# Performance work log

Measured on AMD Instinct MI355X. Metric: run time of the kernel, lower is better.

The kernel has to match this reference:

```python
import jax, jax.numpy as jnp
import numpy as np

CUTOFF = 4          # lattice cutoff radius (module init arg)
NMAX = 64           # padded max neighbors per mobile site (~58 actual at cutoff=4)
BATCH = 131072      # number of independent configurations
B_SOFT = 0.01       # softening constant b in vint
FAR = 1e6           # padding position, masked out


def _rot(c):
    return np.array([[np.cos(c), -np.sin(c)], [np.sin(c), np.cos(c)]])


def _build_geometry():
    """Replicates PotEnergy1P.__init__ (with the intended, bug-fixed math)."""
    s3 = np.sqrt(3.0)
    base = [np.array([0.5, s3 / 6]), np.array([1.0, -s3 / 3]),
            np.array([1.5, s3 / 6]), np.array([1.0, 2 * s3 / 3])]
    mobile = base \
        + [_rot(2 * np.pi / 3) @ p for p in base] \
        + [_rot(4 * np.pi / 3) @ p for p in base]
    mobile = np.stack(mobile)                      # [12, 2]

    def ntopos(n1, n2):
        return np.array([0.5, s3 / 6]) + n1 * np.array([1.0, 0.0]) \
            + n2 * np.array([-0.5, s3 / 2])

    rng = range(-4 * CUTOFF, 4 * CUTOFF)
    grid = np.array([ntopos(n1, n2) for n1 in rng for n2 in rng])  # [G, 2]
    dist = np.linalg.norm(grid[:, None, :] - mobile[None, :, :], axis=-1)  # [G, 12]
    not_mobile = ~np.any(np.isclose(dist, 0.0, atol=1e-8), axis=1)        # [G]

    neighbors = np.full((12, NMAX, 2), FAR, dtype=np.float32)
    mask = np.zeros((12, NMAX), dtype=np.float32)
    for i in range(12):
        idx = np.where(not_mobile & (dist[:, i] < CUTOFF))[0]
        k = len(idx)
        assert k <= NMAX
        neighbors[i, :k] = grid[idx]
        mask[i, :k] = 1.0
    return neighbors, mask


def setup_inputs() -> dict:
    key = jax.random.key(0)
    x = jax.random.normal(key, (BATCH, 24), dtype=jnp.float32)
    neighbors, mask = _build_geometry()
    return {"x": x,
            "neighbors": jnp.asarray(neighbors),
            "mask": jnp.asarray(mask)}


def reference(x, neighbors, mask):
    # x: [B, 24] -> [B, 12, 2] mobile positions
    xr = x.reshape(x.shape[0], -1, 2)
    # pairwise displacement to all padded neighbors: [B, 12, NMAX, 2]
    d = xr[:, :, None, :] - neighbors[None, :, :, :]
    r = jnp.sqrt(jnp.sum(d * d, axis=-1))          # [B, 12, NMAX]
    v = jnp.exp(-r) / (r + B_SOFT)                 # vint with a=1.0, b=0.01
    return jnp.sum(v * mask[None], axis=(1, 2))    # [B] total potential energy
```

## Files before the change

### kernel.cpp

```cpp
#include <hip/hip_runtime.h>

#define NMAX   64
#define NSITES 12
#define SPLIT  4
#define BLOCK  256
#define ROWS   66

#define LOG2E  1.44269504088896340736f
#define LN2    0.69314718055994530942f
#define B_SOFT 0.01f
#define PAD_C  2.0e6f

__global__ __launch_bounds__(BLOCK, 8)
void pot_energy_kernel(const float* __restrict__ x,
                       const float* __restrict__ neighbors,
                       const float* __restrict__ mask,
                       float* __restrict__ out, int B) {
    __shared__ float2 nb[NSITES * ROWS];
    __shared__ int    cnt[NSITES];

    const int tid  = threadIdx.x;
    const int wv   = tid >> 6;
    const int lane = tid & 63;

    for (int idx = tid; idx < NSITES * ROWS; idx += BLOCK)
        nb[idx] = make_float2(PAD_C, PAD_C);
    __syncthreads();

    for (int s = wv; s < NSITES; s += 4) {
        const bool keep = mask[s * NMAX + lane] > 0.5f;
        const unsigned long long bal = __ballot(keep);
        if (keep) {
            const int pos = __popcll(bal & ((1ull << lane) - 1ull));
            const float2 p = ((const float2*)neighbors)[s * NMAX + lane];
            nb[s * ROWS + pos] = make_float2(p.x * LOG2E, p.y * LOG2E);
        }
        if (lane == 0) cnt[s] = __popcll(bal);
    }
    __syncthreads();

    int m = 0;
    #pragma unroll
    for (int s = 0; s < NSITES; ++s) m = max(m, cnt[s]);
    m = (__builtin_amdgcn_readfirstlane(m) + 3) & ~3;

    const int gtid = blockIdx.x * BLOCK + tid;
    const int e = gtid >> 2;
    const int q = gtid & 3;
    if (e >= B) return;

    const float2* xp = (const float2*)(x + (size_t)gtid * 6);
    const float2 p0 = xp[0], p1 = xp[1], p2 = xp[2];
    const float xs_[3] = { p0.x * LOG2E, p1.x * LOG2E, p2.x * LOG2E };
    const float ys_[3] = { p0.y * LOG2E, p1.y * LOG2E, p2.y * LOG2E };

    float acc0 = 0.f, acc1 = 0.f;
    #pragma unroll
    for (int s = 0; s < 3; ++s) {
        const int site = q * 3 + s;
        const float xs = xs_[s];
        const float ys = ys_[s];
        const float4* __restrict__ row4 = (const float4*)&nb[site * ROWS];
        #pragma unroll 2
        for (int j0 = 0; j0 < m; j0 += 4) {
            const float4 ab = row4[(j0 >> 1) + 0];
            const float4 cd = row4[(j0 >> 1) + 1];
            const float nx[4] = { ab.x, ab.z, cd.x, cd.z };
            const float ny[4] = { ab.y, ab.w, cd.y, cd.w };
            float exv[4], dv[4];
            #pragma unroll
            for (int k = 0; k < 4; ++k) {
                const float dx = xs - nx[k];
                const float dy = ys - ny[k];
                const float r2 = fmaf(dy, dy, dx * dx);
                const float rp = __builtin_amdgcn_sqrtf(r2);
                exv[k] = __builtin_amdgcn_exp2f(-rp);
                dv[k]  = fmaf(rp, LN2, B_SOFT);
            }
            const float p01 = dv[0] * dv[1];
            const float p23 = dv[2] * dv[3];
            const float R   = __builtin_amdgcn_rcpf(p01 * p23);
            const float t01 = p23 * R;
            const float t23 = p01 * R;
            acc0 = fmaf(exv[0] * dv[1], t01, acc0);
            acc1 = fmaf(exv[1] * dv[0], t01, acc1);
            acc0 = fmaf(exv[2] * dv[3], t23, acc0);
            acc1 = fmaf(exv[3] * dv[2], t23, acc1);
        }
    }

    float acc = acc0 + acc1;
    acc += __shfl_xor(acc, 1);
    acc += __shfl_xor(acc, 2);
    if (q == 0) out[e] = acc;
}

extern "C" void kernel_launch(void* const* d_in, const int* in_sizes, int n_in,
                              void* d_out, int out_size, void* d_ws, size_t ws_size,
                              hipStream_t stream) {
    const float* x   = (const float*)d_in[0];
    const float* nbr = (const float*)d_in[1];
    const float* msk = (const float*)d_in[2];
    float* out = (float*)d_out;

    const int B = in_sizes[0] / 24;
    const int total_threads = B * SPLIT;
    const int blocks = (total_threads + BLOCK - 1) / BLOCK;
    pot_energy_kernel<<<blocks, BLOCK, 0, stream>>>(x, nbr, msk, out, B);
}
```

Baseline: 86.51 us.

## Replace per-pair exp/sqrt/rcp with piecewise-linear LDS table indexed by r² bits

Builds a per-block shared-memory table of linear segments of exp(-r)/(r+b) as a function of r², indexed by the top float bits of r², and accumulates intercept and slope·r² instead of evaluating sqrt, exp and reciprocal per pair. Neighbor coordinates move to separate x/y arrays and the log2e prescaling is dropped. This aims to remove transcendental-unit pressure from the inner loop, at the cost of random LDS gathers with possible bank conflicts, per-block table setup, and a small approximation error versus the exact function.

```diff
diff --git a/kernel.cpp b/kernel.cpp
--- a/kernel.cpp
+++ b/kernel.cpp
@@ -4,27 +4,50 @@
 #define NSITES 12
 #define SPLIT  4
 #define BLOCK  256
-#define ROWS   66
+#define RS     68
 
-#define LOG2E  1.44269504088896340736f
-#define LN2    0.69314718055994530942f
 #define B_SOFT 0.01f
-#define PAD_C  2.0e6f
+#define PAD_C  4.0e4f
+#define R2_MAX 248.0f
+#define TBL_LO 1392
+#define TBL_N  768
+
+__device__ __forceinline__ float f_exact(float r2) {
+    const float r = sqrtf(r2);
+    return expf(-r) / (r + B_SOFT);
+}
 
 __global__ __launch_bounds__(BLOCK, 8)
 void pot_energy_kernel(const float* __restrict__ x,
                        const float* __restrict__ neighbors,
                        const float* __restrict__ mask,
                        float* __restrict__ out, int B) {
-    __shared__ float2 nb[NSITES * ROWS];
+    __shared__ float  nbx[NSITES][RS];
+    __shared__ float  nby[NSITES][RS];
+    __shared__ float2 tbl[TBL_N];
     __shared__ int    cnt[NSITES];
 
     const int tid  = threadIdx.x;
     const int wv   = tid >> 6;
     const int lane = tid & 63;
 
-    for (int idx = tid; idx < NSITES * ROWS; idx += BLOCK)
-        nb[idx] = make_float2(PAD_C, PAD_C);
+    for (int i = tid; i < TBL_N; i += BLOCK) {
+        const unsigned ii = (unsigned)(i + TBL_LO);
+        const float b0 = __builtin_bit_cast(float, ii << 19);
+        const float b1 = __builtin_bit_cast(float, (ii + 1u) << 19);
+        const float f0 = f_exact(b0);
+        const float f1 = f_exact(b1);
+        const float fm = f_exact(0.5f * (b0 + b1));
+        const float s  = (f1 - f0) / (b1 - b0);
+        const float c  = f0 - s * b0 - 0.5f * (0.5f * (f0 + f1) - fm);
+        tbl[i] = make_float2(c, s);
+    }
+
+    for (int idx = tid; idx < NSITES * RS; idx += BLOCK) {
+        const int s = idx / RS, j = idx - s * RS;
+        nbx[s][j] = PAD_C;
+        nby[s][j] = PAD_C;
+    }
     __syncthreads();
 
     for (int s = wv; s < NSITES; s += 4) {
@@ -33,7 +56,8 @@
         if (keep) {
             const int pos = __popcll(bal & ((1ull << lane) - 1ull));
             const float2 p = ((const float2*)neighbors)[s * NMAX + lane];
-            nb[s * ROWS + pos] = make_float2(p.x * LOG2E, p.y * LOG2E);
+            nbx[s][pos] = p.x;
+            nby[s][pos] = p.y;
         }
         if (lane == 0) cnt[s] = __popcll(bal);
     }
@@ -51,45 +75,40 @@
 
     const float2* xp = (const float2*)(x + (size_t)gtid * 6);
     const float2 p0 = xp[0], p1 = xp[1], p2 = xp[2];
-    const float xs_[3] = { p0.x * LOG2E, p1.x * LOG2E, p2.x * LOG2E };
-    const float ys_[3] = { p0.y * LOG2E, p1.y * LOG2E, p2.y * LOG2E };
+    const float xs_[3] = { p0.x, p1.x, p2.x };
+    const float ys_[3] = { p0.y, p1.y, p2.y };
 
-    float acc0 = 0.f, acc1 = 0.f;
+    float accC = 0.f, accS = 0.f;
     #pragma unroll
     for (int s = 0; s < 3; ++s) {
         const int site = q * 3 + s;
         const float xs = xs_[s];
         const float ys = ys_[s];
-        const float4* __restrict__ row4 = (const float4*)&nb[site * ROWS];
+        const float* __restrict__ rx = nbx[site];
+        const float* __restrict__ ry = nby[site];
         #pragma unroll 2
         for (int j0 = 0; j0 < m; j0 += 4) {
-            const float4 ab = row4[(j0 >> 1) + 0];
-            const float4 cd = row4[(j0 >> 1) + 1];
-            const float nx[4] = { ab.x, ab.z, cd.x, cd.z };
-            const float ny[4] = { ab.y, ab.w, cd.y, cd.w };
-            float exv[4], dv[4];
+            const float4 nx4 = *(const float4*)(rx + j0);
+            const float4 ny4 = *(const float4*)(ry + j0);
+            const float nx[4] = { nx4.x, nx4.y, nx4.z, nx4.w };
+            const float ny[4] = { ny4.x, ny4.y, ny4.z, ny4.w };
             #pragma unroll
             for (int k = 0; k < 4; ++k) {
                 const float dx = xs - nx[k];
                 const float dy = ys - ny[k];
-                const float r2 = fmaf(dy, dy, dx * dx);
-                const float rp = __builtin_amdgcn_sqrtf(r2);
-                exv[k] = __builtin_amdgcn_exp2f(-rp);
-                dv[k]  = fmaf(rp, LN2, B_SOFT);
+                float r2 = fmaf(dy, dy, dx * dx);
+                r2 = fminf(r2, R2_MAX);
+                const unsigned bits = __builtin_bit_cast(unsigned, r2);
+                int idx = (int)(bits >> 19) - TBL_LO;
+                idx = idx < 0 ? 0 : idx;
+                const float2 cs = tbl[idx];
+                accC += cs.x;
+                accS = fmaf(cs.y, r2, accS);
             }
-            const float p01 = dv[0] * dv[1];
-            const float p23 = dv[2] * dv[3];
-            const float R   = __builtin_amdgcn_rcpf(p01 * p23);
-            const float t01 = p23 * R;
-            const float t23 = p01 * R;
-            acc0 = fmaf(exv[0] * dv[1], t01, acc0);
-            acc1 = fmaf(exv[1] * dv[0], t01, acc1);
-            acc0 = fmaf(exv[2] * dv[3], t23, acc0);
-            acc1 = fmaf(exv[3] * dv[2], t23, acc1);
         }
     }
 
-    float acc = acc0 + acc1;
+    float acc = accC + accS;
     acc += __shfl_xor(acc, 1);
     acc += __shfl_xor(acc, 2);
     if (q == 0) out[e] = acc;
```

New measurement: 83.39 us. 1.04x faster.
